# Optimization experiments

Hardware: AMD Instinct MI355X
Metric: run time of the kernel (lower is better)

Reference implementation:

```python
import jax, jax.numpy as jnp
import numpy as np


def setup_inputs() -> dict:
    key = jax.random.key(0)
    ks = jax.random.split(key, 8)
    n_videos, emb_dim = 200000, 128
    n_nodes, k_neigh = 20000, 32
    sc = 1.0 / np.sqrt(emb_dim)
    return {
        "video_embeddings": jax.random.normal(ks[0], (n_videos, emb_dim), jnp.float32),
        "video_nodes": jax.random.randint(ks[1], (n_nodes,), 0, n_videos, jnp.int64 if jax.config.jax_enable_x64 else jnp.int32),
        "neigh_idx": jax.random.randint(ks[2], (n_nodes, k_neigh), 0, n_videos, jnp.int64 if jax.config.jax_enable_x64 else jnp.int32),
        "W1": jax.random.normal(ks[3], (2 * emb_dim, emb_dim), jnp.float32) * sc,
        "b1": jnp.zeros((emb_dim,), jnp.float32),
        "W2": jax.random.normal(ks[4], (emb_dim, emb_dim), jnp.float32) * sc,
        "b2": jnp.zeros((emb_dim,), jnp.float32),
        "W3": jax.random.normal(ks[5], (emb_dim, 1), jnp.float32) * sc,
        "b3": jnp.zeros((1,), jnp.float32),
    }


def reference(video_embeddings, video_nodes, neigh_idx, W1, b1, W2, b2, W3, b3):
    # Ragged per-node loop vectorized as a padded [N, K] neighbor gather.
    neigh_emb = video_embeddings[neigh_idx]          # [N, K, D]
    node_emb = video_embeddings[video_nodes]         # [N, D]
    n, k, d = neigh_emb.shape
    # Attention MLP: cat(neigh, node_repeated) -> relu -> relu -> scalar score
    x = jnp.concatenate([neigh_emb, jnp.broadcast_to(node_emb[:, None, :], (n, k, d))], axis=-1)  # [N, K, 2D]
    h = jax.nn.relu(jnp.einsum("nke,ed->nkd", x, W1) + b1)
    h = jax.nn.relu(jnp.einsum("nke,ed->nkd", h, W2) + b2)
    scores = (jnp.einsum("nkd,do->nko", h, W3) + b3)[..., 0]  # [N, K]
    att = jax.nn.softmax(scores, axis=-1)                      # softmax over neighbors
    # Weighted aggregation: embed_matrix[i] = neigh_emb[i].T @ att[i]
    return jnp.einsum("nkd,nk->nd", neigh_emb, att)
```

## Files before the change

kernel.cpp:

```cpp
#include <hip/hip_runtime.h>
#include <hip/hip_bf16.h>

#define D  128
#define KN 32

typedef __attribute__((ext_vector_type(8))) short bf16x8;
typedef __attribute__((ext_vector_type(4))) float f32x4;

static __device__ __forceinline__ unsigned short f2bf(float f) {
    union { float f; unsigned int u; } v; v.f = f;
    unsigned int u = v.u;
    u += 0x7fff + ((u >> 16) & 1);
    return (unsigned short)(u >> 16);
}
static __device__ __forceinline__ float bf2f(unsigned short h) {
    union { float f; unsigned int u; } v; v.u = ((unsigned int)h) << 16;
    return v.f;
}

__global__ __launch_bounds__(256) void wt_kernel(
    const float* __restrict__ W1, const float* __restrict__ W2,
    unsigned short* __restrict__ W1Tt, unsigned short* __restrict__ W1Tb,
    unsigned short* __restrict__ W2T)
{
    int idx = blockIdx.x * 256 + threadIdx.x;
    if (idx < D * D) {
        int col = idx >> 7, e = idx & 127;
        W1Tt[col * D + e] = f2bf(W1[e * D + col]);
        W1Tb[col * D + e] = f2bf(W1[(D + e) * D + col]);
        W2T [col * D + e] = f2bf(W2[e * D + col]);
    }
}

__global__ __launch_bounds__(256) void p1q_kernel(
    const float* __restrict__ emb, const int* __restrict__ gidx, int M,
    const unsigned short* __restrict__ WT, const float* __restrict__ bias,
    unsigned short* __restrict__ dst, unsigned short* __restrict__ EB)
{
    __shared__ unsigned short sA[128][136];

    const int tid  = threadIdx.x;
    const int lane = tid & 63;
    const int w    = tid >> 6;
    const int m    = lane & 15, q = lane >> 4;
    const int r0   = blockIdx.x * 128;

#pragma unroll
    for (int i = 0; i < 16; ++i) {
        int e = tid + 256 * i;
        int row = e >> 5, c4 = (e & 31) << 2;
        int r = r0 + row; if (r > M - 1) r = M - 1;
        int vr = gidx ? gidx[r] : r;
        const float4 f = *(const float4*)(emb + (long)vr * D + c4);
        ushort4 h;
        h.x = f2bf(f.x); h.y = f2bf(f.y); h.z = f2bf(f.z); h.w = f2bf(f.w);
        *(ushort4*)(&sA[row][c4]) = h;
    }
    __syncthreads();

    if (EB) {
        int row = tid >> 1, half = tid & 1;
        if (r0 + row < M) {
#pragma unroll
            for (int j = 0; j < 8; ++j)
                *(bf16x8*)(EB + (long)(r0 + row) * D + half * 64 + j * 8) =
                    *(const bf16x8*)(&sA[row][half * 64 + j * 8]);
        }
    }

    bf16x8 Bf[2][4];
#pragma unroll
    for (int nt = 0; nt < 2; ++nt)
#pragma unroll
        for (int kk = 0; kk < 4; ++kk)
            Bf[nt][kk] = *(const bf16x8*)(WT + (32 * w + 16 * nt + m) * D + kk * 32 + q * 8);
    float bv[2];
#pragma unroll
    for (int nt = 0; nt < 2; ++nt) bv[nt] = bias ? bias[32 * w + 16 * nt + m] : 0.f;

    f32x4 acc[8][2];
#pragma unroll
    for (int mt = 0; mt < 8; ++mt)
#pragma unroll
        for (int nt = 0; nt < 2; ++nt) acc[mt][nt] = (f32x4){0.f, 0.f, 0.f, 0.f};

#pragma unroll
    for (int kk = 0; kk < 4; ++kk) {
#pragma unroll
        for (int mt = 0; mt < 8; ++mt) {
            bf16x8 a = *(const bf16x8*)(&sA[16 * mt + m][kk * 32 + q * 8]);
            acc[mt][0] = __builtin_amdgcn_mfma_f32_16x16x32_bf16(a, Bf[0][kk], acc[mt][0], 0, 0, 0);
            acc[mt][1] = __builtin_amdgcn_mfma_f32_16x16x32_bf16(a, Bf[1][kk], acc[mt][1], 0, 0, 0);
        }
    }

#pragma unroll
    for (int mt = 0; mt < 8; ++mt)
#pragma unroll
        for (int nt = 0; nt < 2; ++nt) {
            int col = 32 * w + 16 * nt + m;
#pragma unroll
            for (int r = 0; r < 4; ++r) {
                int row = r0 + 16 * mt + 4 * q + r;
                if (row < M) dst[(long)row * D + col] = f2bf(acc[mt][nt][r] + bv[nt]);
            }
        }
}

template <bool USE_EB>
__global__ __launch_bounds__(256, 3) void agg_kernel(
    const float* __restrict__ emb, const unsigned short* __restrict__ EB,
    const int* __restrict__ nidx,
    const unsigned short* __restrict__ W2T,
    const float* __restrict__ b2, const float* __restrict__ W3,
    const float* __restrict__ b3,
    const unsigned short* __restrict__ P1, const unsigned short* __restrict__ Q,
    float* __restrict__ out, int NN)
{
    __shared__ unsigned short sX[128][136];
    __shared__ int   sIdx[128];
    __shared__ float sSp[4][128];
    __shared__ float sAtt[128];

    const int tid  = threadIdx.x;
    const int lane = tid & 63;
    const int w    = tid >> 6;
    const int m    = lane & 15, q = lane >> 4;

    bf16x8 Bf[2][4];
#pragma unroll
    for (int nt = 0; nt < 2; ++nt)
#pragma unroll
        for (int kk = 0; kk < 4; ++kk)
            Bf[nt][kk] = *(const bf16x8*)(W2T + (32 * w + 16 * nt + m) * D + kk * 32 + q * 8);
    float b2v[2], w3v[2];
#pragma unroll
    for (int nt = 0; nt < 2; ++nt) {
        int col = 32 * w + 16 * nt + m;
        b2v[nt] = b2[col];
        w3v[nt] = W3[col];
    }
    const float b3s = b3[0];

    const int groups = (NN + 3) >> 2;
    for (int g = blockIdx.x; g < groups; g += gridDim.x) {
        const int node0 = g * 4;

        {
            int row = tid >> 1, half = tid & 1;
            int nd = node0 + (row >> 5); if (nd > NN - 1) nd = NN - 1;
            int k = row & 31;
            int ni = nidx[nd * KN + k];
            if (half == 0) sIdx[row] = ni;
            const bf16x8* pp = (const bf16x8*)(P1 + (long)ni * D) + half * 8;
            const bf16x8* qq = (const bf16x8*)(Q + (long)nd * D) + half * 8;
#pragma unroll
            for (int j = 0; j < 8; ++j) {
                bf16x8 p = pp[j], qv = qq[j], r;
#pragma unroll
                for (int h = 0; h < 8; ++h) {
                    float v = bf2f((unsigned short)p[h]) + bf2f((unsigned short)qv[h]);
                    r[h] = (short)f2bf(v > 0.f ? v : 0.f);
                }
                *(bf16x8*)(&sX[row][half * 64 + j * 8]) = r;
            }
        }
        __syncthreads();

        bf16x8 gv[8];
        if (USE_EB) {
#pragma unroll
            for (int j = 0; j < 8; ++j) {
                int k = (lane >> 4) + 4 * j;
                int ni = sIdx[w * KN + k];
                gv[j] = *(const bf16x8*)(EB + (long)ni * D + (lane & 15) * 8);
            }
        }

        f32x4 acc[8][2];
#pragma unroll
        for (int mt = 0; mt < 8; ++mt)
#pragma unroll
            for (int nt = 0; nt < 2; ++nt) acc[mt][nt] = (f32x4){0.f, 0.f, 0.f, 0.f};

#pragma unroll
        for (int kk = 0; kk < 4; ++kk) {
#pragma unroll
            for (int mt = 0; mt < 8; ++mt) {
                bf16x8 a = *(const bf16x8*)(&sX[16 * mt + m][kk * 32 + q * 8]);
                acc[mt][0] = __builtin_amdgcn_mfma_f32_16x16x32_bf16(a, Bf[0][kk], acc[mt][0], 0, 0, 0);
                acc[mt][1] = __builtin_amdgcn_mfma_f32_16x16x32_bf16(a, Bf[1][kk], acc[mt][1], 0, 0, 0);
            }
        }

#pragma unroll
        for (int mt = 0; mt < 8; ++mt) {
            float p[4];
#pragma unroll
            for (int r = 0; r < 4; ++r) {
                float h0 = acc[mt][0][r] + b2v[0]; h0 = h0 > 0.f ? h0 : 0.f;
                float h1 = acc[mt][1][r] + b2v[1]; h1 = h1 > 0.f ? h1 : 0.f;
                p[r] = h0 * w3v[0] + h1 * w3v[1];
            }
#pragma unroll
            for (int off = 8; off >= 1; off >>= 1)
#pragma unroll
                for (int r = 0; r < 4; ++r) p[r] += __shfl_xor(p[r], off, 16);
            if (m == 0) {
#pragma unroll
                for (int r = 0; r < 4; ++r) sSp[w][16 * mt + 4 * q + r] = p[r];
            }
        }
        __syncthreads();

        if (tid < 128) {
            float s = sSp[0][tid] + sSp[1][tid] + sSp[2][tid] + sSp[3][tid] + b3s;
            float mx = s;
#pragma unroll
            for (int off = 16; off >= 1; off >>= 1) mx = fmaxf(mx, __shfl_xor(mx, off, 32));
            float e = __expf(s - mx);
            float sum = e;
#pragma unroll
            for (int off = 16; off >= 1; off >>= 1) sum += __shfl_xor(sum, off, 32);
            sAtt[tid] = e / sum;
        }
        __syncthreads();

        if (USE_EB) {
            float r[8] = {0.f, 0.f, 0.f, 0.f, 0.f, 0.f, 0.f, 0.f};
#pragma unroll
            for (int j = 0; j < 8; ++j) {
                float a = sAtt[w * KN + (lane >> 4) + 4 * j];
#pragma unroll
                for (int h = 0; h < 8; ++h)
                    r[h] += a * bf2f((unsigned short)gv[j][h]);
            }
#pragma unroll
            for (int h = 0; h < 8; ++h) {
                r[h] += __shfl_xor(r[h], 16);
                r[h] += __shfl_xor(r[h], 32);
            }
            int nd = node0 + w;
            if (lane < 16 && nd < NN) {
                float4 o0 = {r[0], r[1], r[2], r[3]};
                float4 o1 = {r[4], r[5], r[6], r[7]};
                *(float4*)(out + (long)nd * D + lane * 8)     = o0;
                *(float4*)(out + (long)nd * D + lane * 8 + 4) = o1;
            }
        } else {
            float a0 = 0.f, a1 = 0.f;
            for (int k = 0; k < KN; ++k) {
                float att = sAtt[w * KN + k];
                const float* er = emb + (long)sIdx[w * KN + k] * D;
                a0 += att * er[lane];
                a1 += att * er[lane + 64];
            }
            int nd = node0 + w;
            if (nd < NN) {
                out[(long)nd * D + lane]      = a0;
                out[(long)nd * D + lane + 64] = a1;
            }
        }
        __syncthreads();
    }
}

__global__ __launch_bounds__(128) void naive_kernel(
    const float* __restrict__ emb, const int* __restrict__ vnodes,
    const int* __restrict__ nidx,
    const float* __restrict__ W1, const float* __restrict__ b1,
    const float* __restrict__ W2, const float* __restrict__ b2,
    const float* __restrict__ W3, const float* __restrict__ b3,
    float* __restrict__ out)
{
    __shared__ float sE[KN + 1][D];
    __shared__ float sH[KN][D];
    __shared__ float sH2[KN][D];
    __shared__ float sS[KN];
    __shared__ float sA2[KN];
    const int node = blockIdx.x, tid = threadIdx.x;

    for (int r = 0; r < KN + 1; ++r) {
        int vr = (r < KN) ? nidx[node * KN + r] : vnodes[node];
        sE[r][tid] = emb[(long)vr * D + tid];
    }
    __syncthreads();
    for (int k = 0; k < KN; ++k) {
        float s = b1[tid];
        for (int e = 0; e < D; ++e) s += sE[k][e]  * W1[e * D + tid];
        for (int e = 0; e < D; ++e) s += sE[KN][e] * W1[(D + e) * D + tid];
        sH[k][tid] = s > 0.f ? s : 0.f;
    }
    __syncthreads();
    for (int k = 0; k < KN; ++k) {
        float s = b2[tid];
        for (int e = 0; e < D; ++e) s += sH[k][e] * W2[e * D + tid];
        sH2[k][tid] = s > 0.f ? s : 0.f;
    }
    __syncthreads();
    if (tid < KN) {
        float s = b3[0];
        for (int e = 0; e < D; ++e) s += sH2[tid][e] * W3[e];
        sS[tid] = s;
    }
    __syncthreads();
    if (tid == 0) {
        float mx = sS[0];
        for (int k = 1; k < KN; ++k) mx = fmaxf(mx, sS[k]);
        float sum = 0.f;
        for (int k = 0; k < KN; ++k) { sA2[k] = __expf(sS[k] - mx); sum += sA2[k]; }
        for (int k = 0; k < KN; ++k) sA2[k] /= sum;
    }
    __syncthreads();
    float a = 0.f;
    for (int k = 0; k < KN; ++k) a += sA2[k] * sE[k][tid];
    out[(long)node * D + tid] = a;
}

extern "C" void kernel_launch(void* const* d_in, const int* in_sizes, int n_in,
                              void* d_out, int out_size, void* d_ws, size_t ws_size,
                              hipStream_t stream) {
    const float* emb    = (const float*)d_in[0];
    const int*   vnodes = (const int*)d_in[1];
    const int*   nidx   = (const int*)d_in[2];
    const float* W1     = (const float*)d_in[3];
    const float* b1     = (const float*)d_in[4];
    const float* W2     = (const float*)d_in[5];
    const float* b2     = (const float*)d_in[6];
    const float* W3     = (const float*)d_in[7];
    const float* b3     = (const float*)d_in[8];
    float* out = (float*)d_out;

    const int NV = in_sizes[0] / D;
    const int NN = in_sizes[1];

    const size_t p1_elems = (size_t)NV * D;
    const size_t q_elems  = (size_t)NN * D;
    const size_t wt_elems = (size_t)D * D;
    const size_t base_elems = p1_elems + q_elems + 3 * wt_elems;
    const size_t need_base = base_elems * sizeof(unsigned short);
    const size_t need_eb   = (base_elems + p1_elems) * sizeof(unsigned short);

    if (ws_size >= need_base) {
        unsigned short* P1   = (unsigned short*)d_ws;
        unsigned short* Q    = P1 + p1_elems;
        unsigned short* W1Tt = Q + q_elems;
        unsigned short* W1Tb = W1Tt + wt_elems;
        unsigned short* W2T  = W1Tb + wt_elems;
        unsigned short* EB   = (ws_size >= need_eb) ? (W2T + wt_elems) : nullptr;

        wt_kernel<<<(D * D + 255) / 256, 256, 0, stream>>>(W1, W2, W1Tt, W1Tb, W2T);
        p1q_kernel<<<(NV + 127) / 128, 256, 0, stream>>>(emb, nullptr, NV, W1Tt, nullptr, P1, EB);
        p1q_kernel<<<(NN + 127) / 128, 256, 0, stream>>>(emb, vnodes, NN, W1Tb, b1, Q, nullptr);
        if (EB)
            agg_kernel<true><<<2048, 256, 0, stream>>>(emb, EB, nidx, W2T, b2, W3, b3, P1, Q, out, NN);
        else
            agg_kernel<false><<<2048, 256, 0, stream>>>(emb, nullptr, nidx, W2T, b2, W3, b3, P1, Q, out, NN);
    } else {
        naive_kernel<<<NN, D, 0, stream>>>(emb, vnodes, nidx, W1, b1, W2, b2, W3, b3, out);
    }
}
```

Baseline: 315.4 us.

## Merge P1/Q launches, software-prefetch P1 rows, drop trailing sync in aggregation

Merges the two p1q launches into a single grid whose block index picks the P1 (all videos) or Q (node) path, which removes one launch and its tail. In agg_kernel, the next group's neighbor indices and P1 rows are loaded into registers while the current group's MFMA and softmax run, so gather latency overlaps compute. The trailing __syncthreads at the end of each loop iteration is removed, and the kernel moves from 2048 blocks with launch_bounds min-blocks 3 to 1024 blocks with min-blocks 2 to make room for the extra prefetch registers. The fp32-embedding fallback path is dropped, and EB is now always required. Removing the end-of-loop barrier risks sIdx/sAtt being overwritten while another wave is still reading them.

```diff
diff --git a/kernel.cpp b/kernel.cpp
--- a/kernel.cpp
+++ b/kernel.cpp
@@ -33,9 +33,12 @@
 }
 
 __global__ __launch_bounds__(256) void p1q_kernel(
-    const float* __restrict__ emb, const int* __restrict__ gidx, int M,
-    const unsigned short* __restrict__ WT, const float* __restrict__ bias,
-    unsigned short* __restrict__ dst, unsigned short* __restrict__ EB)
+    const float* __restrict__ emb, const int* __restrict__ vnodes,
+    int NV, int NN, int nvBlocks,
+    const unsigned short* __restrict__ W1Tt, const unsigned short* __restrict__ W1Tb,
+    const float* __restrict__ b1,
+    unsigned short* __restrict__ P1, unsigned short* __restrict__ Q,
+    unsigned short* __restrict__ EB)
 {
     __shared__ unsigned short sA[128][136];
 
@@ -43,14 +46,20 @@
     const int lane = tid & 63;
     const int w    = tid >> 6;
     const int m    = lane & 15, q = lane >> 4;
-    const int r0   = blockIdx.x * 128;
+
+    const bool nv = (int)blockIdx.x < nvBlocks;
+    const int  bi = nv ? blockIdx.x : blockIdx.x - nvBlocks;
+    const int  M  = nv ? NV : NN;
+    const unsigned short* WT = nv ? W1Tt : W1Tb;
+    unsigned short* dst = nv ? P1 : Q;
+    const int r0 = bi * 128;
 
 #pragma unroll
     for (int i = 0; i < 16; ++i) {
         int e = tid + 256 * i;
         int row = e >> 5, c4 = (e & 31) << 2;
         int r = r0 + row; if (r > M - 1) r = M - 1;
-        int vr = gidx ? gidx[r] : r;
+        int vr = nv ? r : vnodes[r];
         const float4 f = *(const float4*)(emb + (long)vr * D + c4);
         ushort4 h;
         h.x = f2bf(f.x); h.y = f2bf(f.y); h.z = f2bf(f.z); h.w = f2bf(f.w);
@@ -58,7 +67,7 @@
     }
     __syncthreads();
 
-    if (EB) {
+    if (nv) {
         int row = tid >> 1, half = tid & 1;
         if (r0 + row < M) {
 #pragma unroll
@@ -76,7 +85,7 @@
             Bf[nt][kk] = *(const bf16x8*)(WT + (32 * w + 16 * nt + m) * D + kk * 32 + q * 8);
     float bv[2];
 #pragma unroll
-    for (int nt = 0; nt < 2; ++nt) bv[nt] = bias ? bias[32 * w + 16 * nt + m] : 0.f;
+    for (int nt = 0; nt < 2; ++nt) bv[nt] = nv ? 0.f : b1[32 * w + 16 * nt + m];
 
     f32x4 acc[8][2];
 #pragma unroll
@@ -107,13 +116,10 @@
         }
 }
 
-template <bool USE_EB>
-__global__ __launch_bounds__(256, 3) void agg_kernel(
-    const float* __restrict__ emb, const unsigned short* __restrict__ EB,
-    const int* __restrict__ nidx,
-    const unsigned short* __restrict__ W2T,
-    const float* __restrict__ b2, const float* __restrict__ W3,
-    const float* __restrict__ b3,
+__global__ __launch_bounds__(256, 2) void agg_kernel(
+    const unsigned short* __restrict__ EB, const int* __restrict__ nidx,
+    const unsigned short* __restrict__ W2T, const float* __restrict__ b2,
+    const float* __restrict__ W3, const float* __restrict__ b3,
     const unsigned short* __restrict__ P1, const unsigned short* __restrict__ Q,
     float* __restrict__ out, int NN)
 {
@@ -126,6 +132,7 @@
     const int lane = tid & 63;
     const int w    = tid >> 6;
     const int m    = lane & 15, q = lane >> 4;
+    const int row  = tid >> 1, half = tid & 1;
 
     bf16x8 Bf[2][4];
 #pragma unroll
@@ -143,38 +150,58 @@
     const float b3s = b3[0];
 
     const int groups = (NN + 3) >> 2;
-    for (int g = blockIdx.x; g < groups; g += gridDim.x) {
+
+    int g = blockIdx.x;
+    int ni_cur = 0;
+    bf16x8 pf[8];
+    if (g < groups) {
+        int nd = g * 4 + (row >> 5); if (nd > NN - 1) nd = NN - 1;
+        ni_cur = nidx[nd * KN + (row & 31)];
+#pragma unroll
+        for (int j = 0; j < 8; ++j)
+            pf[j] = *(const bf16x8*)(P1 + (long)ni_cur * D + half * 64 + j * 8);
+    }
+
+    for (; g < groups; g += gridDim.x) {
         const int node0 = g * 4;
-
+        int nd = node0 + (row >> 5); if (nd > NN - 1) nd = NN - 1;
+
+        if (half == 0) sIdx[row] = ni_cur;
         {
-            int row = tid >> 1, half = tid & 1;
-            int nd = node0 + (row >> 5); if (nd > NN - 1) nd = NN - 1;
-            int k = row & 31;
-            int ni = nidx[nd * KN + k];
-            if (half == 0) sIdx[row] = ni;
-            const bf16x8* pp = (const bf16x8*)(P1 + (long)ni * D) + half * 8;
             const bf16x8* qq = (const bf16x8*)(Q + (long)nd * D) + half * 8;
 #pragma unroll
             for (int j = 0; j < 8; ++j) {
-                bf16x8 p = pp[j], qv = qq[j], r;
+                bf16x8 qv = qq[j], r;
 #pragma unroll
                 for (int h = 0; h < 8; ++h) {
-                    float v = bf2f((unsigned short)p[h]) + bf2f((unsigned short)qv[h]);
+                    float v = bf2f((unsigned short)pf[j][h]) + bf2f((unsigned short)qv[h]);
                     r[h] = (short)f2bf(v > 0.f ? v : 0.f);
                 }
                 *(bf16x8*)(&sX[row][half * 64 + j * 8]) = r;
             }
         }
+
+        const int gn = g + gridDim.x;
+        const bool more = gn < groups;
+        int ni_next = ni_cur;
+        if (more) {
+            int ndn = gn * 4 + (row >> 5); if (ndn > NN - 1) ndn = NN - 1;
+            ni_next = nidx[ndn * KN + (row & 31)];
+        }
         __syncthreads();
 
         bf16x8 gv[8];
-        if (USE_EB) {
-#pragma unroll
-            for (int j = 0; j < 8; ++j) {
-                int k = (lane >> 4) + 4 * j;
-                int ni = sIdx[w * KN + k];
-                gv[j] = *(const bf16x8*)(EB + (long)ni * D + (lane & 15) * 8);
-            }
+#pragma unroll
+        for (int j = 0; j < 8; ++j) {
+            int k = (lane >> 4) + 4 * j;
+            int ik = sIdx[w * KN + k];
+            gv[j] = *(const bf16x8*)(EB + (long)ik * D + (lane & 15) * 8);
+        }
+
+        if (more) {
+#pragma unroll
+            for (int j = 0; j < 8; ++j)
+                pf[j] = *(const bf16x8*)(P1 + (long)ni_next * D + half * 64 + j * 8);
         }
 
         f32x4 acc[8][2];
@@ -226,7 +253,7 @@
         }
         __syncthreads();
 
-        if (USE_EB) {
+        {
             float r[8] = {0.f, 0.f, 0.f, 0.f, 0.f, 0.f, 0.f, 0.f};
 #pragma unroll
             for (int j = 0; j < 8; ++j) {
@@ -240,28 +267,15 @@
                 r[h] += __shfl_xor(r[h], 16);
                 r[h] += __shfl_xor(r[h], 32);
             }
-            int nd = node0 + w;
-            if (lane < 16 && nd < NN) {
+            int ndw = node0 + w;
+            if (lane < 16 && ndw < NN) {
                 float4 o0 = {r[0], r[1], r[2], r[3]};
                 float4 o1 = {r[4], r[5], r[6], r[7]};
-                *(float4*)(out + (long)nd * D + lane * 8)     = o0;
-                *(float4*)(out + (long)nd * D + lane * 8 + 4) = o1;
-            }
-        } else {
-            float a0 = 0.f, a1 = 0.f;
-            for (int k = 0; k < KN; ++k) {
-                float att = sAtt[w * KN + k];
-                const float* er = emb + (long)sIdx[w * KN + k] * D;
-                a0 += att * er[lane];
-                a1 += att * er[lane + 64];
-            }
-            int nd = node0 + w;
-            if (nd < NN) {
-                out[(long)nd * D + lane]      = a0;
-                out[(long)nd * D + lane + 64] = a1;
-            }
-        }
-        __syncthreads();
+                *(float4*)(out + (long)ndw * D + lane * 8)     = o0;
+                *(float4*)(out + (long)ndw * D + lane * 8 + 4) = o1;
+            }
+        }
+        ni_cur = ni_next;
     }
 }
 
@@ -337,25 +351,24 @@
     const size_t p1_elems = (size_t)NV * D;
     const size_t q_elems  = (size_t)NN * D;
     const size_t wt_elems = (size_t)D * D;
-    const size_t base_elems = p1_elems + q_elems + 3 * wt_elems;
-    const size_t need_base = base_elems * sizeof(unsigned short);
-    const size_t need_eb   = (base_elems + p1_elems) * sizeof(unsigned short);
-
-    if (ws_size >= need_base) {
+    const size_t need = (2 * p1_elems + q_elems + 3 * wt_elems) * sizeof(unsigned short);
+
+    if (ws_size >= need) {
         unsigned short* P1   = (unsigned short*)d_ws;
         unsigned short* Q    = P1 + p1_elems;
         unsigned short* W1Tt = Q + q_elems;
         unsigned short* W1Tb = W1Tt + wt_elems;
         unsigned short* W2T  = W1Tb + wt_elems;
-        unsigned short* EB   = (ws_size >= need_eb) ? (W2T + wt_elems) : nullptr;
+        unsigned short* EB   = W2T + wt_elems;
+
+        const int nvBlocks = (NV + 127) / 128;
+        const int qBlocks  = (NN + 127) / 128;
 
         wt_kernel<<<(D * D + 255) / 256, 256, 0, stream>>>(W1, W2, W1Tt, W1Tb, W2T);
-        p1q_kernel<<<(NV + 127) / 128, 256, 0, stream>>>(emb, nullptr, NV, W1Tt, nullptr, P1, EB);
-        p1q_kernel<<<(NN + 127) / 128, 256, 0, stream>>>(emb, vnodes, NN, W1Tb, b1, Q, nullptr);
-        if (EB)
-            agg_kernel<true><<<2048, 256, 0, stream>>>(emb, EB, nidx, W2T, b2, W3, b3, P1, Q, out, NN);
-        else
-            agg_kernel<false><<<2048, 256, 0, stream>>>(emb, nullptr, nidx, W2T, b2, W3, b3, P1, Q, out, NN);
+        p1q_kernel<<<nvBlocks + qBlocks, 256, 0, stream>>>(
+            emb, vnodes, NV, NN, nvBlocks, W1Tt, W1Tb, b1, P1, Q, EB);
+        agg_kernel<<<1024, 256, 0, stream>>>(
+            EB, nidx, W2T, b2, W3, b3, P1, Q, out, NN);
     } else {
         naive_kernel<<<NN, D, 0, stream>>>(emb, vnodes, nidx, W1, b1, W2, b2, W3, b3, out);
     }
```

After: 303.2 us. 1.04x faster.

## Compute first MLP layer on gathered neighbors instead of precomputing all videos

Applied to the files above, without the earlier changes.

Drops the precompute of the first MLP layer over all 200k video embeddings (and the bf16 embedding copy). The agg kernel now gathers the 640k neighbor rows, converts them to bf16 in shared memory and runs the W1-top GEMM per tile, adding the node term Q, now kept in fp32. This trades a full-table GEMM plus its bf16 writes and reads for about 3x more MFMA work on gathered rows, with extra LDS traffic and syncs. The final weighted sum now uses bf16-rounded neighbor embeddings taken from shared memory.

```diff
diff --git a/kernel.cpp b/kernel.cpp
--- a/kernel.cpp
+++ b/kernel.cpp
@@ -3,6 +3,7 @@
 
 #define D  128
 #define KN 32
+#define LST 136
 
 typedef __attribute__((ext_vector_type(8))) short bf16x8;
 typedef __attribute__((ext_vector_type(4))) float f32x4;
@@ -16,6 +17,12 @@
 static __device__ __forceinline__ float bf2f(unsigned short h) {
     union { float f; unsigned int u; } v; v.u = ((unsigned int)h) << 16;
     return v.f;
+}
+static __device__ __forceinline__ unsigned int pk2bf(float a, float b) {
+    float2 t; t.x = a; t.y = b;
+    __hip_bfloat162 h = __float22bfloat162_rn(t);
+    union { __hip_bfloat162 h; unsigned int u; } v; v.h = h;
+    return v.u;
 }
 
 __global__ __launch_bounds__(256) void wt_kernel(
@@ -32,12 +39,12 @@
     }
 }
 
-__global__ __launch_bounds__(256) void p1q_kernel(
-    const float* __restrict__ emb, const int* __restrict__ gidx, int M,
-    const unsigned short* __restrict__ WT, const float* __restrict__ bias,
-    unsigned short* __restrict__ dst, unsigned short* __restrict__ EB)
+__global__ __launch_bounds__(256) void q_kernel(
+    const float* __restrict__ emb, const int* __restrict__ vnodes, int NN,
+    const unsigned short* __restrict__ W1Tb, const float* __restrict__ b1,
+    float* __restrict__ Qf)
 {
-    __shared__ unsigned short sA[128][136];
+    __shared__ unsigned short sA[128][LST];
 
     const int tid  = threadIdx.x;
     const int lane = tid & 63;
@@ -49,8 +56,8 @@
     for (int i = 0; i < 16; ++i) {
         int e = tid + 256 * i;
         int row = e >> 5, c4 = (e & 31) << 2;
-        int r = r0 + row; if (r > M - 1) r = M - 1;
-        int vr = gidx ? gidx[r] : r;
+        int r = r0 + row; if (r > NN - 1) r = NN - 1;
+        int vr = vnodes[r];
         const float4 f = *(const float4*)(emb + (long)vr * D + c4);
         ushort4 h;
         h.x = f2bf(f.x); h.y = f2bf(f.y); h.z = f2bf(f.z); h.w = f2bf(f.w);
@@ -58,25 +65,15 @@
     }
     __syncthreads();
 
-    if (EB) {
-        int row = tid >> 1, half = tid & 1;
-        if (r0 + row < M) {
-#pragma unroll
-            for (int j = 0; j < 8; ++j)
-                *(bf16x8*)(EB + (long)(r0 + row) * D + half * 64 + j * 8) =
-                    *(const bf16x8*)(&sA[row][half * 64 + j * 8]);
-        }
-    }
-
     bf16x8 Bf[2][4];
 #pragma unroll
     for (int nt = 0; nt < 2; ++nt)
 #pragma unroll
         for (int kk = 0; kk < 4; ++kk)
-            Bf[nt][kk] = *(const bf16x8*)(WT + (32 * w + 16 * nt + m) * D + kk * 32 + q * 8);
+            Bf[nt][kk] = *(const bf16x8*)(W1Tb + (32 * w + 16 * nt + m) * D + kk * 32 + q * 8);
     float bv[2];
 #pragma unroll
-    for (int nt = 0; nt < 2; ++nt) bv[nt] = bias ? bias[32 * w + 16 * nt + m] : 0.f;
+    for (int nt = 0; nt < 2; ++nt) bv[nt] = b1[32 * w + 16 * nt + m];
 
     f32x4 acc[8][2];
 #pragma unroll
@@ -85,14 +82,13 @@
         for (int nt = 0; nt < 2; ++nt) acc[mt][nt] = (f32x4){0.f, 0.f, 0.f, 0.f};
 
 #pragma unroll
-    for (int kk = 0; kk < 4; ++kk) {
+    for (int kk = 0; kk < 4; ++kk)
 #pragma unroll
         for (int mt = 0; mt < 8; ++mt) {
             bf16x8 a = *(const bf16x8*)(&sA[16 * mt + m][kk * 32 + q * 8]);
             acc[mt][0] = __builtin_amdgcn_mfma_f32_16x16x32_bf16(a, Bf[0][kk], acc[mt][0], 0, 0, 0);
             acc[mt][1] = __builtin_amdgcn_mfma_f32_16x16x32_bf16(a, Bf[1][kk], acc[mt][1], 0, 0, 0);
         }
-    }
 
 #pragma unroll
     for (int mt = 0; mt < 8; ++mt)
@@ -102,23 +98,20 @@
 #pragma unroll
             for (int r = 0; r < 4; ++r) {
                 int row = r0 + 16 * mt + 4 * q + r;
-                if (row < M) dst[(long)row * D + col] = f2bf(acc[mt][nt][r] + bv[nt]);
-            }
-        }
-}
-
-template <bool USE_EB>
+                if (row < NN) Qf[(long)row * D + col] = acc[mt][nt][r] + bv[nt];
+            }
+        }
+}
+
 __global__ __launch_bounds__(256, 3) void agg_kernel(
-    const float* __restrict__ emb, const unsigned short* __restrict__ EB,
-    const int* __restrict__ nidx,
-    const unsigned short* __restrict__ W2T,
+    const float* __restrict__ emb, const int* __restrict__ nidx,
+    const unsigned short* __restrict__ W1Tt, const unsigned short* __restrict__ W2T,
     const float* __restrict__ b2, const float* __restrict__ W3,
-    const float* __restrict__ b3,
-    const unsigned short* __restrict__ P1, const unsigned short* __restrict__ Q,
+    const float* __restrict__ b3, const float* __restrict__ Qf,
     float* __restrict__ out, int NN)
 {
-    __shared__ unsigned short sX[128][136];
-    __shared__ int   sIdx[128];
+    __shared__ unsigned short sU[128][LST];
+    __shared__ float sQf[4][D];
     __shared__ float sSp[4][128];
     __shared__ float sAtt[128];
 
@@ -127,12 +120,14 @@
     const int w    = tid >> 6;
     const int m    = lane & 15, q = lane >> 4;
 
-    bf16x8 Bf[2][4];
-#pragma unroll
-    for (int nt = 0; nt < 2; ++nt)
-#pragma unroll
-        for (int kk = 0; kk < 4; ++kk)
-            Bf[nt][kk] = *(const bf16x8*)(W2T + (32 * w + 16 * nt + m) * D + kk * 32 + q * 8);
+    bf16x8 Af[2][4], Bf[2][4];
+#pragma unroll
+    for (int t = 0; t < 2; ++t)
+#pragma unroll
+        for (int kk = 0; kk < 4; ++kk) {
+            Af[t][kk] = *(const bf16x8*)(W1Tt + (32 * w + 16 * t + m) * D + kk * 32 + q * 8);
+            Bf[t][kk] = *(const bf16x8*)(W2T  + (32 * w + 16 * t + m) * D + kk * 32 + q * 8);
+        }
     float b2v[2], w3v[2];
 #pragma unroll
     for (int nt = 0; nt < 2; ++nt) {
@@ -147,35 +142,71 @@
         const int node0 = g * 4;
 
         {
+            int i2 = tid * 2, nd = i2 >> 7, c = i2 & 127;
+            int ndg = node0 + nd; if (ndg > NN - 1) ndg = NN - 1;
+            *(float2*)(&sQf[nd][c]) = *(const float2*)(Qf + (long)ndg * D + c);
+        }
+        {
             int row = tid >> 1, half = tid & 1;
-            int nd = node0 + (row >> 5); if (nd > NN - 1) nd = NN - 1;
-            int k = row & 31;
-            int ni = nidx[nd * KN + k];
-            if (half == 0) sIdx[row] = ni;
-            const bf16x8* pp = (const bf16x8*)(P1 + (long)ni * D) + half * 8;
-            const bf16x8* qq = (const bf16x8*)(Q + (long)nd * D) + half * 8;
+            int ndg = node0 + (row >> 5); if (ndg > NN - 1) ndg = NN - 1;
+            int ni = nidx[ndg * KN + (row & 31)];
+            const float* src = emb + (long)ni * D + half * 64;
 #pragma unroll
             for (int j = 0; j < 8; ++j) {
-                bf16x8 p = pp[j], qv = qq[j], r;
-#pragma unroll
-                for (int h = 0; h < 8; ++h) {
-                    float v = bf2f((unsigned short)p[h]) + bf2f((unsigned short)qv[h]);
-                    r[h] = (short)f2bf(v > 0.f ? v : 0.f);
+                float4 f0 = *(const float4*)(src + j * 8);
+                float4 f1 = *(const float4*)(src + j * 8 + 4);
+                uint4 pk;
+                pk.x = pk2bf(f0.x, f0.y); pk.y = pk2bf(f0.z, f0.w);
+                pk.z = pk2bf(f1.x, f1.y); pk.w = pk2bf(f1.z, f1.w);
+                *(uint4*)(&sU[row][half * 64 + j * 8]) = pk;
+            }
+        }
+        __syncthreads();
+
+        bf16x8 gv[8];
+#pragma unroll
+        for (int j = 0; j < 8; ++j)
+            gv[j] = *(const bf16x8*)(&sU[w * KN + (lane >> 4) + 4 * j][(lane & 15) * 8]);
+
+        f32x4 acc1[4][2][2];
+#pragma unroll
+        for (int nd = 0; nd < 4; ++nd)
+#pragma unroll
+            for (int t = 0; t < 2; ++t)
+#pragma unroll
+                for (int nt = 0; nt < 2; ++nt) acc1[nd][t][nt] = (f32x4){0.f, 0.f, 0.f, 0.f};
+
+#pragma unroll
+        for (int nd = 0; nd < 4; ++nd)
+#pragma unroll
+            for (int kk = 0; kk < 4; ++kk) {
+                bf16x8 e0 = *(const bf16x8*)(&sU[nd * 32 + m][kk * 32 + q * 8]);
+                bf16x8 e1 = *(const bf16x8*)(&sU[nd * 32 + 16 + m][kk * 32 + q * 8]);
+                acc1[nd][0][0] = __builtin_amdgcn_mfma_f32_16x16x32_bf16(Af[0][kk], e0, acc1[nd][0][0], 0, 0, 0);
+                acc1[nd][1][0] = __builtin_amdgcn_mfma_f32_16x16x32_bf16(Af[1][kk], e0, acc1[nd][1][0], 0, 0, 0);
+                acc1[nd][0][1] = __builtin_amdgcn_mfma_f32_16x16x32_bf16(Af[0][kk], e1, acc1[nd][0][1], 0, 0, 0);
+                acc1[nd][1][1] = __builtin_amdgcn_mfma_f32_16x16x32_bf16(Af[1][kk], e1, acc1[nd][1][1], 0, 0, 0);
+            }
+        __syncthreads();
+
+#pragma unroll
+        for (int nd = 0; nd < 4; ++nd)
+#pragma unroll
+            for (int t = 0; t < 2; ++t) {
+                int xc = 32 * w + 16 * t + 4 * q;
+                float q0 = sQf[nd][xc], q1 = sQf[nd][xc + 1];
+                float q2 = sQf[nd][xc + 2], q3 = sQf[nd][xc + 3];
+#pragma unroll
+                for (int nt = 0; nt < 2; ++nt) {
+                    float v0 = fmaxf(acc1[nd][t][nt][0] + q0, 0.f);
+                    float v1 = fmaxf(acc1[nd][t][nt][1] + q1, 0.f);
+                    float v2 = fmaxf(acc1[nd][t][nt][2] + q2, 0.f);
+                    float v3 = fmaxf(acc1[nd][t][nt][3] + q3, 0.f);
+                    uint2 pk; pk.x = pk2bf(v0, v1); pk.y = pk2bf(v2, v3);
+                    *(uint2*)(&sU[nd * 32 + 16 * nt + m][xc]) = pk;
                 }
-                *(bf16x8*)(&sX[row][half * 64 + j * 8]) = r;
-            }
-        }
-        __syncthreads();
-
-        bf16x8 gv[8];
-        if (USE_EB) {
-#pragma unroll
-            for (int j = 0; j < 8; ++j) {
-                int k = (lane >> 4) + 4 * j;
-                int ni = sIdx[w * KN + k];
-                gv[j] = *(const bf16x8*)(EB + (long)ni * D + (lane & 15) * 8);
-            }
-        }
+            }
+        __syncthreads();
 
         f32x4 acc[8][2];
 #pragma unroll
@@ -184,14 +215,13 @@
             for (int nt = 0; nt < 2; ++nt) acc[mt][nt] = (f32x4){0.f, 0.f, 0.f, 0.f};
 
 #pragma unroll
-        for (int kk = 0; kk < 4; ++kk) {
+        for (int kk = 0; kk < 4; ++kk)
 #pragma unroll
             for (int mt = 0; mt < 8; ++mt) {
-                bf16x8 a = *(const bf16x8*)(&sX[16 * mt + m][kk * 32 + q * 8]);
+                bf16x8 a = *(const bf16x8*)(&sU[16 * mt + m][kk * 32 + q * 8]);
                 acc[mt][0] = __builtin_amdgcn_mfma_f32_16x16x32_bf16(a, Bf[0][kk], acc[mt][0], 0, 0, 0);
                 acc[mt][1] = __builtin_amdgcn_mfma_f32_16x16x32_bf16(a, Bf[1][kk], acc[mt][1], 0, 0, 0);
             }
-        }
 
 #pragma unroll
         for (int mt = 0; mt < 8; ++mt) {
@@ -226,7 +256,7 @@
         }
         __syncthreads();
 
-        if (USE_EB) {
+        {
             float r[8] = {0.f, 0.f, 0.f, 0.f, 0.f, 0.f, 0.f, 0.f};
 #pragma unroll
             for (int j = 0; j < 8; ++j) {
@@ -240,28 +270,14 @@
                 r[h] += __shfl_xor(r[h], 16);
                 r[h] += __shfl_xor(r[h], 32);
             }
-            int nd = node0 + w;
-            if (lane < 16 && nd < NN) {
+            int ndw = node0 + w;
+            if (lane < 16 && ndw < NN) {
                 float4 o0 = {r[0], r[1], r[2], r[3]};
                 float4 o1 = {r[4], r[5], r[6], r[7]};
-                *(float4*)(out + (long)nd * D + lane * 8)     = o0;
-                *(float4*)(out + (long)nd * D + lane * 8 + 4) = o1;
-            }
-        } else {
-            float a0 = 0.f, a1 = 0.f;
-            for (int k = 0; k < KN; ++k) {
-                float att = sAtt[w * KN + k];
-                const float* er = emb + (long)sIdx[w * KN + k] * D;
-                a0 += att * er[lane];
-                a1 += att * er[lane + 64];
-            }
-            int nd = node0 + w;
-            if (nd < NN) {
-                out[(long)nd * D + lane]      = a0;
-                out[(long)nd * D + lane + 64] = a1;
-            }
-        }
-        __syncthreads();
+                *(float4*)(out + (long)ndw * D + lane * 8)     = o0;
+                *(float4*)(out + (long)ndw * D + lane * 8 + 4) = o1;
+            }
+        }
     }
 }
 
@@ -331,31 +347,22 @@
     const float* b3     = (const float*)d_in[8];
     float* out = (float*)d_out;
 
-    const int NV = in_sizes[0] / D;
     const int NN = in_sizes[1];
 
-    const size_t p1_elems = (size_t)NV * D;
-    const size_t q_elems  = (size_t)NN * D;
+    const size_t q_bytes  = (size_t)NN * D * sizeof(float);
     const size_t wt_elems = (size_t)D * D;
-    const size_t base_elems = p1_elems + q_elems + 3 * wt_elems;
-    const size_t need_base = base_elems * sizeof(unsigned short);
-    const size_t need_eb   = (base_elems + p1_elems) * sizeof(unsigned short);
-
-    if (ws_size >= need_base) {
-        unsigned short* P1   = (unsigned short*)d_ws;
-        unsigned short* Q    = P1 + p1_elems;
-        unsigned short* W1Tt = Q + q_elems;
+    const size_t need = q_bytes + 3 * wt_elems * sizeof(unsigned short);
+
+    if (ws_size >= need) {
+        float* Qf            = (float*)d_ws;
+        unsigned short* W1Tt = (unsigned short*)((char*)d_ws + q_bytes);
         unsigned short* W1Tb = W1Tt + wt_elems;
         unsigned short* W2T  = W1Tb + wt_elems;
-        unsigned short* EB   = (ws_size >= need_eb) ? (W2T + wt_elems) : nullptr;
 
         wt_kernel<<<(D * D + 255) / 256, 256, 0, stream>>>(W1, W2, W1Tt, W1Tb, W2T);
-        p1q_kernel<<<(NV + 127) / 128, 256, 0, stream>>>(emb, nullptr, NV, W1Tt, nullptr, P1, EB);
-        p1q_kernel<<<(NN + 127) / 128, 256, 0, stream>>>(emb, vnodes, NN, W1Tb, b1, Q, nullptr);
-        if (EB)
-            agg_kernel<true><<<2048, 256, 0, stream>>>(emb, EB, nidx, W2T, b2, W3, b3, P1, Q, out, NN);
-        else
-            agg_kernel<false><<<2048, 256, 0, stream>>>(emb, nullptr, nidx, W2T, b2, W3, b3, P1, Q, out, NN);
+        q_kernel<<<(NN + 127) / 128, 256, 0, stream>>>(emb, vnodes, NN, W1Tb, b1, Qf);
+        agg_kernel<<<2048, 256, 0, stream>>>(
+            emb, nidx, W1Tt, W2T, b2, W3, b3, Qf, out, NN);
     } else {
         naive_kernel<<<NN, D, 0, stream>>>(emb, vnodes, nidx, W1, b1, W2, b2, W3, b3, out);
     }
```

Result: slower. 336.0 us (+6.5%).
